# Kernel tuning notes

Measured on AMD Instinct MI355X. Metric: run time of the kernel, lower is better.

## Reference

```python
import jax, jax.numpy as jnp
import numpy as np

TAU = 1.0       # softmax_temp
SOS_IDX = 1
EOS_IDX = 2
MAX_LEN = 20    # total message length incl. SOS/EOS -> 18 decode steps


def setup_inputs() -> dict:
    key = jax.random.key(0)
    ks = jax.random.split(key, 12)
    B, E, H, V, F = 512, 256, 512, 4096, 512
    T = MAX_LEN - 2
    s = lambda k, shape, sc: jax.random.normal(k, shape, jnp.float32) * sc
    return {
        "proto_a": s(ks[0], (B, F), 1.0),
        "proto_b": s(ks[1], (B, F), 1.0),
        "W_init": s(ks[2], (H, 2 * F), (2 * F) ** -0.5),
        "b_init": jnp.zeros((H,), jnp.float32),
        "W_ih": s(ks[3], (3 * H, E), E ** -0.5),
        "W_hh": s(ks[4], (3 * H, H), H ** -0.5),
        "b_ih": jnp.zeros((3 * H,), jnp.float32),
        "b_hh": jnp.zeros((3 * H,), jnp.float32),
        "W_out": s(ks[5], (V, H), H ** -0.5),
        "b_out": jnp.zeros((V,), jnp.float32),
        "emb": s(ks[6], (V, E), 1.0),
        # uniforms in (0,1) turned into Gumbel noise inside reference
        "u_gumbel": jax.random.uniform(ks[7], (T, B, V), jnp.float32, 1e-6, 1.0 - 1e-6),
    }


def reference(proto_a, proto_b, W_init, b_init, W_ih, W_hh, b_ih, b_hh,
              W_out, b_out, emb, u_gumbel):
    B = proto_a.shape[0]
    V = W_out.shape[0]
    # init_h(cat(prototypes, 1)) -> h0 [B, H]
    h0 = jnp.concatenate([proto_a, proto_b], axis=1) @ W_init.T + b_init
    sos = jnp.zeros((B, V), h0.dtype).at[:, SOS_IDX].set(1.0)
    eos = jnp.zeros((B, V), h0.dtype).at[:, EOS_IDX].set(1.0)
    x0 = sos @ emb  # [B, E]
    g = -jnp.log(-jnp.log(u_gumbel))  # Gumbel(0,1) noise, [T, B, V]

    def step(carry, gt):
        h, x = carry  # h [B,H], x [B,E]
        # PyTorch single-step GRU cell
        gi = x @ W_ih.T + b_ih
        gh = h @ W_hh.T + b_hh
        ir, iz, inn = jnp.split(gi, 3, axis=-1)
        hr, hz, hn = jnp.split(gh, 3, axis=-1)
        r = jax.nn.sigmoid(ir + hr)
        z = jax.nn.sigmoid(iz + hz)
        n = jnp.tanh(inn + r * hn)
        h_new = (1.0 - z) * n + z * h
        logits = h_new @ W_out.T + b_out  # [B, V]
        # gumbel_softmax(tau, hard=False) then straight-through hard one-hot
        y = jax.nn.softmax((logits + gt) / TAU, axis=-1)
        hard = jax.nn.one_hot(jnp.argmax(y, axis=-1), V, dtype=y.dtype)
        onehot = hard - jax.lax.stop_gradient(y) + y
        return (h_new, onehot @ emb), onehot

    _, toks = jax.lax.scan(step, (h0, x0), g)  # toks [T, B, V]
    lang = jnp.concatenate([sos[:, None], jnp.swapaxes(toks, 0, 1), eos[:, None]], axis=1)
    return lang  # [B, MAX_LEN, V]
```

## Files before the change

kernel.cpp:

```cpp
#include <hip/hip_runtime.h>
#include <hip/hip_bf16.h>
#include <math.h>

#define B_ 512
#define E_ 256
#define H_ 512
#define V_ 4096
#define T_ 18
#define L_ 20
#define MARGIN_ 0.04f
#define CCAP_ 64

typedef __attribute__((ext_vector_type(8))) short bf16x8;
typedef __attribute__((ext_vector_type(4))) float f32x4;

__global__ __launch_bounds__(256) void kprep32(const float* __restrict__ pa,
                                               const float* __restrict__ pb,
                                               const float* __restrict__ Wout,
                                               float* __restrict__ cat,
                                               __hip_bfloat16* __restrict__ WB) {
  int idx = blockIdx.x * 256 + threadIdx.x;
  if (idx < 131072) {
    int e0 = idx * 4;
    int b = e0 >> 10, k = e0 & 1023;
    float4 v = (k < 512) ? *reinterpret_cast<const float4*>(pa + (size_t)b * 512 + k)
                         : *reinterpret_cast<const float4*>(pb + (size_t)b * 512 + (k - 512));
    *reinterpret_cast<float4*>(cat + e0) = v;
  } else {
    int e0 = (idx - 131072) * 4;
    float4 w = *reinterpret_cast<const float4*>(Wout + e0);
    __hip_bfloat16 b0 = __float2bfloat16(w.x), b1 = __float2bfloat16(w.y);
    __hip_bfloat16 b2 = __float2bfloat16(w.z), b3 = __float2bfloat16(w.w);
    ushort4 o;
    o.x = *reinterpret_cast<unsigned short*>(&b0);
    o.y = *reinterpret_cast<unsigned short*>(&b1);
    o.z = *reinterpret_cast<unsigned short*>(&b2);
    o.w = *reinterpret_cast<unsigned short*>(&b3);
    *reinterpret_cast<ushort4*>(WB + e0) = o;
  }
}

__device__ __forceinline__ void gemm64_body(const float* __restrict__ A,
                                            const float* __restrict__ W,
                                            float* __restrict__ P,
                                            int N, int lda, int kPer,
                                            int bx, int by, int bz, int My,
                                            int tid, char* smemRaw) {
  float (*As)[130] = reinterpret_cast<float(*)[130]>(smemRaw);
  float (*Bs)[68]  = reinterpret_cast<float(*)[68]>(smemRaw + 8320);
  const int tx = tid & 15, ty = tid >> 4;
  const int bn = bx * 64, bm = by * 128;
  const int k0 = bz * kPer;
  const size_t pOff = (size_t)bz * My * 128 * N;
  const int kk0 = tid & 15;
  const int ra0 = (tid >> 4) * 8;
  const int cb0 = (tid >> 4) * 4;

  float acc[8][4] = {};
  for (int kb = 0; kb < kPer; kb += 16) {
#pragma unroll
    for (int q = 0; q < 8; ++q)
      As[kk0][ra0 + q] = A[(size_t)(bm + ra0 + q) * lda + k0 + kb + kk0];
#pragma unroll
    for (int q = 0; q < 4; ++q)
      Bs[kk0][cb0 + q] = W[(size_t)(bn + cb0 + q) * lda + k0 + kb + kk0];
    __syncthreads();
#pragma unroll
    for (int kk = 0; kk < 16; ++kk) {
      float a[8], b[4];
#pragma unroll
      for (int i = 0; i < 8; ++i) a[i] = As[kk][ty + 16 * i];
#pragma unroll
      for (int j = 0; j < 4; ++j) b[j] = Bs[kk][tx + 16 * j];
#pragma unroll
      for (int i = 0; i < 8; ++i)
#pragma unroll
        for (int j = 0; j < 4; ++j) acc[i][j] = fmaf(a[i], b[j], acc[i][j]);
    }
    __syncthreads();
  }
#pragma unroll
  for (int i = 0; i < 8; ++i) {
    size_t r = (size_t)(bm + ty + 16 * i);
#pragma unroll
    for (int j = 0; j < 4; ++j)
      P[pOff + r * N + bn + tx + 16 * j] = acc[i][j];
  }
}

__global__ __launch_bounds__(256) void setupGemms(const float* __restrict__ cat,
                                                  const float* __restrict__ Winit,
                                                  float* __restrict__ h0P,
                                                  const float* __restrict__ emb,
                                                  const float* __restrict__ Wih,
                                                  float* __restrict__ giP) {
  __shared__ __align__(16) char smemRaw[12672];
  const int bid = blockIdx.x, tid = threadIdx.x;
  if (bid < 256) {
    int bx = bid & 7, by = (bid >> 3) & 3, bz = bid >> 5;
    gemm64_body(cat, Winit, h0P, 512, 1024, 128, bx, by, bz, 4, tid, smemRaw);
  } else {
    int gid = bid - 256;
    int bx = gid % 24, by = gid / 24;
    gemm64_body(emb, Wih, giP, 1536, 256, 256, bx, by, 0, 32, tid, smemRaw);
  }
}

__global__ __launch_bounds__(256) void ghK(const float* __restrict__ h,
                                           const float* __restrict__ Whh,
                                           float* __restrict__ ghP) {
  __shared__ __align__(16) char smemRaw[12672];
  const int bid = blockIdx.x, tid = threadIdx.x;
  int bx = bid % 24, by = (bid / 24) & 3, bz = bid / 96;
  gemm64_body(h, Whh, ghP, 1536, 512, 64, bx, by, bz, 4, tid, smemRaw);
}

__global__ __launch_bounds__(256) void reduceH0(const float* __restrict__ parts,
                                                const float* __restrict__ binit,
                                                float* __restrict__ h,
                                                __hip_bfloat16* __restrict__ hB) {
  int i = blockIdx.x * 256 + threadIdx.x;
  double s = (double)binit[i & 511];
#pragma unroll
  for (int c = 0; c < 8; ++c) s += (double)parts[(size_t)c * 262144 + i];
  float f = (float)s;
  h[i] = f;
  hB[i] = __float2bfloat16(f);
}

__device__ __forceinline__ void screen_body(const __hip_bfloat16* __restrict__ hB,
                                            const __hip_bfloat16* __restrict__ WoutB,
                                            float* __restrict__ loP,
                                            int bid, int tid) {
  const int wave = tid >> 6, lane = tid & 63;
  const int bx = bid & 63, by = bid >> 6;
  const int bm = by * 64 + wave * 16;
  const int bn = bx * 64;
  const int rA = lane & 15, g = lane >> 4;
  const __hip_bfloat16* ha = hB + (size_t)(bm + rA) * H_ + g * 8;
  const __hip_bfloat16* wb = WoutB + (size_t)(bn + rA) * H_ + g * 8;
  f32x4 acc[4] = {};
  for (int k0 = 0; k0 < H_; k0 += 32) {
    bf16x8 a = *reinterpret_cast<const bf16x8*>(ha + k0);
#pragma unroll
    for (int j = 0; j < 4; ++j) {
      bf16x8 b = *reinterpret_cast<const bf16x8*>(wb + (size_t)j * 16 * H_ + k0);
      acc[j] = __builtin_amdgcn_mfma_f32_16x16x32_bf16(a, b, acc[j], 0, 0, 0);
    }
  }
#pragma unroll
  for (int j = 0; j < 4; ++j)
#pragma unroll
    for (int r = 0; r < 4; ++r)
      loP[(size_t)(bm + g * 4 + r) * V_ + bn + j * 16 + rA] = acc[j][r];
}

__device__ __forceinline__ int pick_body(const float* __restrict__ loP,
                                         const float* __restrict__ h,
                                         const float* __restrict__ Wout,
                                         const float* __restrict__ bout,
                                         const float* __restrict__ ub,
                                         int bid, int tid, char* smemRaw) {
  double* sd    = reinterpret_cast<double*>(smemRaw);
  int*    pre   = reinterpret_cast<int*>(smemRaw + 2048);
  int*    candV = reinterpret_cast<int*>(smemRaw + 3072);
  float*  swv   = reinterpret_cast<float*>(smemRaw + 3328);
  int*    swi   = reinterpret_cast<int*>(smemRaw + 3344);
  int*    sct   = reinterpret_cast<int*>(smemRaw + 3360);
  double* bestS = reinterpret_cast<double*>(smemRaw + 3376);
  int*    bestV = reinterpret_cast<int*>(smemRaw + 3384);
  const int lane = tid & 63, wv = tid >> 6;
  const float* l0 = loP + (size_t)bid * V_;
  float sloc[16];
  float best = -1e30f; int bi = 0x7fffffff;
#pragma unroll
  for (int i = 0; i < 16; ++i) {
    int v = tid + 256 * i;
    float s = l0[v] + bout[v] - logf(-logf(ub[v]));
    sloc[i] = s;
    if (s > best) { best = s; bi = v; }
  }
#pragma unroll
  for (int off = 1; off < 64; off <<= 1) {
    float ov = __shfl_xor(best, off, 64);
    int   oi = __shfl_xor(bi,  off, 64);
    if (ov > best || (ov == best && oi < bi)) { best = ov; bi = oi; }
  }
  if (lane == 0) { swv[wv] = best; swi[wv] = bi; }
  __syncthreads();
  float smax = swv[0]; int amax = swi[0];
#pragma unroll
  for (int w = 1; w < 4; ++w) {
    float ov = swv[w]; int oi = swi[w];
    if (ov > smax || (ov == smax && oi < amax)) { smax = ov; amax = oi; }
  }
  int c = 0;
#pragma unroll
  for (int i = 0; i < 16; ++i) if (sloc[i] >= smax - MARGIN_) ++c;
  int csum = c;
#pragma unroll
  for (int off = 1; off < 64; off <<= 1) csum += __shfl_xor(csum, off, 64);
  if (lane == 0) sct[wv] = csum;
  __syncthreads();
  int tot = sct[0] + sct[1] + sct[2] + sct[3];

  int tok;
  if (tot == 1) {
    tok = amax;
  } else if (tot <= CCAP_) {
    int lv[16];
    int cc = 0;
#pragma unroll
    for (int i = 0; i < 16; ++i)
      if (sloc[i] >= smax - MARGIN_) { if (cc < 16) lv[cc] = tid + 256 * i; ++cc; }
    pre[tid] = cc;
    __syncthreads();
    for (int off = 1; off < 256; off <<= 1) {
      int vv = (tid >= off) ? pre[tid - off] : 0;
      __syncthreads();
      pre[tid] += vv;
      __syncthreads();
    }
    int base = pre[tid] - cc;
    for (int q = 0; q < cc; ++q) candV[base + q] = lv[q];
    if (tid == 0) { *bestS = -1e300; *bestV = 0x7fffffff; }
    __syncthreads();
    const float* hb = h + (size_t)bid * H_;
    for (int ci = 0; ci < tot; ++ci) {
      int v = candV[ci];
      const float* wr = Wout + (size_t)v * H_;
      double p = (double)hb[tid] * (double)wr[tid]
               + (double)hb[tid + 256] * (double)wr[tid + 256];
#pragma unroll
      for (int off = 1; off < 64; off <<= 1) p += __shfl_xor(p, off, 64);
      if (lane == 0) sd[wv] = p;
      __syncthreads();
      if (tid == 0) {
        double s = sd[0] + sd[1] + sd[2] + sd[3]
                 + (double)bout[v] - log(-log((double)ub[v]));
        if (s > *bestS || (s == *bestS && v < *bestV)) { *bestS = s; *bestV = v; }
      }
      __syncthreads();
    }
    tok = *bestV;
  } else {
    const float* hb = h + (size_t)bid * H_;
    double dbest = -1e300; int dbi = 0x7fffffff;
    for (int i = 0; i < 16; ++i) {
      int v = tid + 256 * i;
      const float* wr = Wout + (size_t)v * H_;
      double dot = 0.0;
      for (int k = 0; k < H_; ++k) dot = fma((double)hb[k], (double)wr[k], dot);
      double s = dot + (double)bout[v] - log(-log((double)ub[v]));
      if (s > dbest) { dbest = s; dbi = v; }
    }
#pragma unroll
    for (int off = 1; off < 64; off <<= 1) {
      double od = __shfl_xor(dbest, off, 64);
      int    oi = __shfl_xor(dbi,  off, 64);
      if (od > dbest || (od == dbest && oi < dbi)) { dbest = od; dbi = oi; }
    }
    if (lane == 0) { sd[wv] = dbest; pre[wv] = dbi; }
    __syncthreads();
    double bs = sd[0]; int bv = pre[0];
#pragma unroll
    for (int w = 1; w < 4; ++w) {
      if (sd[w] > bs || (sd[w] == bs && pre[w] < bv)) { bs = sd[w]; bv = pre[w]; }
    }
    tok = bv;
  }
  return tok;
}

__global__ __launch_bounds__(256) void gates_init(const float* __restrict__ ghP,
                                                  const float* __restrict__ giP,
                                                  const float* __restrict__ bih,
                                                  const float* __restrict__ bhh,
                                                  float* __restrict__ h,
                                                  __hip_bfloat16* __restrict__ hB) {
  const int bid = blockIdx.x, tid = threadIdx.x;
  const float* g0 = giP + (size_t)1 * 1536;
  size_t base = (size_t)bid * 1536;
#pragma unroll
  for (int c = 0; c < 2; ++c) {
    int j = c * 256 + tid;
    int idx = bid * 512 + j;
    double gr = (double)bhh[j], gz = (double)bhh[512 + j], gn = (double)bhh[1024 + j];
#pragma unroll
    for (int s = 0; s < 8; ++s) {
      const float* p = ghP + (size_t)s * 786432 + base;
      gr += (double)p[j]; gz += (double)p[512 + j]; gn += (double)p[1024 + j];
    }
    float ir  = g0[j]        + bih[j];
    float iz  = g0[512 + j]  + bih[512 + j];
    float inn = g0[1024 + j] + bih[1024 + j];
    float r = 1.f / (1.f + expf(-(ir + (float)gr)));
    float z = 1.f / (1.f + expf(-(iz + (float)gz)));
    float n = tanhf(inn + r * (float)gn);
    float hn = (1.f - z) * n + z * h[idx];
    h[idx] = hn;
    hB[idx] = __float2bfloat16(hn);
  }
}

__global__ __launch_bounds__(256) void fusedA(const float* __restrict__ h,
                                              const float* __restrict__ Whh,
                                              const __hip_bfloat16* __restrict__ hB,
                                              const __hip_bfloat16* __restrict__ WoutB,
                                              float* __restrict__ ghP,
                                              float* __restrict__ loP,
                                              int doGemm) {
  __shared__ __align__(16) char smemRaw[12672];
  const int bid = blockIdx.x, tid = threadIdx.x;
  if (bid < 768) {
    if (doGemm) {
      int bx = bid % 24, by = (bid / 24) & 3, bz = bid / 96;
      gemm64_body(h, Whh, ghP, 1536, 512, 64, bx, by, bz, 4, tid, smemRaw);
    }
  } else {
    screen_body(hB, WoutB, loP, bid - 768, tid);
  }
}

__global__ __launch_bounds__(256) void fusedB(const float* __restrict__ loP,
                                              float* __restrict__ h,
                                              const float* __restrict__ Wout,
                                              const float* __restrict__ bout,
                                              const float* __restrict__ u,
                                              const float* __restrict__ ghP,
                                              const float* __restrict__ giP,
                                              const float* __restrict__ bih,
                                              const float* __restrict__ bhh,
                                              __hip_bfloat16* __restrict__ hB,
                                              int* __restrict__ toks,
                                              int t, int doGates) {
  __shared__ __align__(16) char smemRaw[5440];
  const int bid = blockIdx.x, tid = threadIdx.x;
  const int j0 = tid, j1 = 256 + tid;
  double gr0 = (double)bhh[j0], gz0 = (double)bhh[512 + j0], gn0 = (double)bhh[1024 + j0];
  double gr1 = (double)bhh[j1], gz1 = (double)bhh[512 + j1], gn1 = (double)bhh[1024 + j1];
  if (doGates) {
    size_t base = (size_t)bid * 1536;
#pragma unroll
    for (int s = 0; s < 8; ++s) {
      const float* p = ghP + (size_t)s * 786432 + base;
      gr0 += (double)p[j0]; gz0 += (double)p[512 + j0]; gn0 += (double)p[1024 + j0];
      gr1 += (double)p[j1]; gz1 += (double)p[512 + j1]; gn1 += (double)p[1024 + j1];
    }
  }
  const float* ub = u + (size_t)bid * V_;
  int tok = pick_body(loP, h, Wout, bout, ub, bid, tid, smemRaw);
  if (tid == 0) toks[t * B_ + bid] = tok;
  if (doGates) {
    const float* g0 = giP + (size_t)tok * 1536;
    {
      int idx = bid * 512 + j0;
      float ir  = g0[j0]        + bih[j0];
      float iz  = g0[512 + j0]  + bih[512 + j0];
      float inn = g0[1024 + j0] + bih[1024 + j0];
      float r = 1.f / (1.f + expf(-(ir + (float)gr0)));
      float z = 1.f / (1.f + expf(-(iz + (float)gz0)));
      float n = tanhf(inn + r * (float)gn0);
      float hn = (1.f - z) * n + z * h[idx];
      h[idx] = hn;
      hB[idx] = __float2bfloat16(hn);
    }
    {
      int idx = bid * 512 + j1;
      float ir  = g0[j1]        + bih[j1];
      float iz  = g0[512 + j1]  + bih[512 + j1];
      float inn = g0[1024 + j1] + bih[1024 + j1];
      float r = 1.f / (1.f + expf(-(ir + (float)gr1)));
      float z = 1.f / (1.f + expf(-(iz + (float)gz1)));
      float n = tanhf(inn + r * (float)gn1);
      float hn = (1.f - z) * n + z * h[idx];
      h[idx] = hn;
      hB[idx] = __float2bfloat16(hn);
    }
  }
}

__global__ __launch_bounds__(256) void kfinal32(float* __restrict__ out,
                                                const int* __restrict__ toks) {
  size_t c = (size_t)blockIdx.x * 256 + threadIdx.x;
  size_t e0 = c * 4;
  int v0 = (int)(e0 & (size_t)(V_ - 1));
  size_t row = e0 >> 12;
  int p = (int)(row % L_);
  int b = (int)(row / L_);
  int tok;
  if (p == 0)           tok = 1;
  else if (p == L_ - 1) tok = 2;
  else                  tok = toks[(p - 1) * B_ + b];
  float4 val = make_float4(0.f, 0.f, 0.f, 0.f);
  int d = tok - v0;
  if (d >= 0 && d < 4) {
    if (d == 0) val.x = 1.f; else if (d == 1) val.y = 1.f;
    else if (d == 2) val.z = 1.f; else val.w = 1.f;
  }
  reinterpret_cast<float4*>(out)[c] = val;
}

__global__ void kmark_ws(float* out) {
  if (threadIdx.x == 0) out[0] = 16.0f;
}
__global__ void kmark_resolver(float* out) {
  if (threadIdx.x == 0) out[2] = 11.0f;
}

extern "C" void kernel_launch(void* const* d_in, const int* in_sizes, int n_in,
                              void* d_out, int out_size, void* d_ws, size_t ws_size,
                              hipStream_t stream) {
  static const int EXPECT[12] = {262144, 262144, 524288, 512, 393216, 786432,
                                 1536, 1536, 2097152, 4096, 1048576, 37748736};
  const float* R[12];
  bool resolved = (n_in == 12);
  if (resolved) {
    bool used[12] = {};
    for (int i = 0; i < 12; ++i) {
      int f = -1;
      for (int j = 0; j < 12; ++j)
        if (!used[j] && in_sizes[j] == EXPECT[i]) { f = j; break; }
      if (f < 0) { resolved = false; break; }
      used[f] = true;
      R[i] = (const float*)d_in[f];
    }
  }
  if (!resolved)
    for (int i = 0; i < 12 && i < n_in; ++i) R[i] = (const float*)d_in[i];

  const float *pa = R[0], *pb = R[1], *Winit = R[2], *binit = R[3],
              *Wih = R[4], *Whh = R[5], *bih = R[6], *bhh = R[7],
              *Wout = R[8], *bout = R[9], *emb = R[10], *ug = R[11];
  float* out = (float*)d_out;

  const size_t TOK_BYTES = (size_t)T_ * B_ * sizeof(int);
  if (ws_size < TOK_BYTES) { kmark_ws<<<1, 64, 0, stream>>>(out); return; }
  int* toks = (int*)d_ws;

  const size_t SC_FLOATS = 16121856;
  float* sc;
  if (ws_size >= 40960 + SC_FLOATS * sizeof(float)) {
    sc = (float*)((char*)d_ws + 40960);
  } else {
    sc = (float*)d_out;
  }
  float* h    = sc;
  float* giP  = sc + 262144;
  float* ghP  = sc + 6553600;
  float* loP  = sc + 12845056;
  __hip_bfloat16* hB    = (__hip_bfloat16*)(sc + 14942208);
  __hip_bfloat16* WoutB = (__hip_bfloat16*)(sc + 15073280);
  float* cat  = ghP;
  float* h0P  = ghP + 524288;

  kprep32<<<2560, 256, 0, stream>>>(pa, pb, Wout, cat, WoutB);
  setupGemms<<<1024, 256, 0, stream>>>(cat, Winit, h0P, emb, Wih, giP);
  reduceH0<<<1024, 256, 0, stream>>>(h0P, binit, h, hB);
  ghK<<<768, 256, 0, stream>>>(h, Whh, ghP);
  gates_init<<<512, 256, 0, stream>>>(ghP, giP, bih, bhh, h, hB);

  for (int t = 0; t < T_; ++t) {
    const float* uslice = ug + (size_t)t * B_ * V_;
    int notLast = (t < T_ - 1) ? 1 : 0;
    fusedA<<<1280, 256, 0, stream>>>(h, Whh, hB, WoutB, ghP, loP, notLast);
    fusedB<<<512, 256, 0, stream>>>(loP, h, Wout, bout, uslice, ghP, giP,
                                    bih, bhh, hB, toks, t, notLast);
  }

  kfinal32<<<40960, 256, 0, stream>>>(out, toks);
  if (!resolved) kmark_resolver<<<1, 64, 0, stream>>>(out);
}
```

Baseline: 917.6 us.

## Compute recurrent h@W_hh with 3-way bf16-split MFMA instead of fp32 split-K GEMM

Replaces the fp32 SIMT split-K GEMM for the GRU hidden-state projection with a bf16 MFMA kernel that splits h and W_hh into three bf16 terms each and sums six cross products, approximating fp32 precision. W_hh is split once in the prep kernel and h is split in the gate updates. This removes the 8-way split-K partial buffers and the double-precision reduction in the gate kernels, and cuts the GEMM grid from 768 to 192 blocks. The cost is six MFMAs per tile plus triple loads, and precision is slightly reduced, which could flip argmax decisions.

```diff
diff --git a/kernel.cpp b/kernel.cpp
--- a/kernel.cpp
+++ b/kernel.cpp
@@ -14,11 +14,32 @@
 typedef __attribute__((ext_vector_type(8))) short bf16x8;
 typedef __attribute__((ext_vector_type(4))) float f32x4;
 
+__device__ __forceinline__ unsigned short bfbits(float x) {
+  __hip_bfloat16 b = __float2bfloat16(x);
+  return *reinterpret_cast<unsigned short*>(&b);
+}
+__device__ __forceinline__ float bf2f(unsigned short u) {
+  unsigned v = ((unsigned)u) << 16;
+  return *reinterpret_cast<float*>(&v);
+}
+__device__ __forceinline__ void split3(float x, unsigned short& s1,
+                                       unsigned short& s2, unsigned short& s3) {
+  s1 = bfbits(x);
+  float r = x - bf2f(s1);
+  s2 = bfbits(r);
+  float r2 = r - bf2f(s2);
+  s3 = bfbits(r2);
+}
+
 __global__ __launch_bounds__(256) void kprep32(const float* __restrict__ pa,
                                                const float* __restrict__ pb,
                                                const float* __restrict__ Wout,
+                                               const float* __restrict__ Whh,
                                                float* __restrict__ cat,
-                                               __hip_bfloat16* __restrict__ WB) {
+                                               __hip_bfloat16* __restrict__ WB,
+                                               unsigned short* __restrict__ W1,
+                                               unsigned short* __restrict__ W2,
+                                               unsigned short* __restrict__ W3) {
   int idx = blockIdx.x * 256 + threadIdx.x;
   if (idx < 131072) {
     int e0 = idx * 4;
@@ -26,17 +47,23 @@
     float4 v = (k < 512) ? *reinterpret_cast<const float4*>(pa + (size_t)b * 512 + k)
                          : *reinterpret_cast<const float4*>(pb + (size_t)b * 512 + (k - 512));
     *reinterpret_cast<float4*>(cat + e0) = v;
-  } else {
+  } else if (idx < 655360) {
     int e0 = (idx - 131072) * 4;
     float4 w = *reinterpret_cast<const float4*>(Wout + e0);
-    __hip_bfloat16 b0 = __float2bfloat16(w.x), b1 = __float2bfloat16(w.y);
-    __hip_bfloat16 b2 = __float2bfloat16(w.z), b3 = __float2bfloat16(w.w);
     ushort4 o;
-    o.x = *reinterpret_cast<unsigned short*>(&b0);
-    o.y = *reinterpret_cast<unsigned short*>(&b1);
-    o.z = *reinterpret_cast<unsigned short*>(&b2);
-    o.w = *reinterpret_cast<unsigned short*>(&b3);
+    o.x = bfbits(w.x); o.y = bfbits(w.y); o.z = bfbits(w.z); o.w = bfbits(w.w);
     *reinterpret_cast<ushort4*>(WB + e0) = o;
+  } else if (idx < 851968) {
+    int e0 = (idx - 655360) * 4;
+    float4 w = *reinterpret_cast<const float4*>(Whh + e0);
+    ushort4 o1, o2, o3;
+    split3(w.x, o1.x, o2.x, o3.x);
+    split3(w.y, o1.y, o2.y, o3.y);
+    split3(w.z, o1.z, o2.z, o3.z);
+    split3(w.w, o1.w, o2.w, o3.w);
+    *reinterpret_cast<ushort4*>(W1 + e0) = o1;
+    *reinterpret_cast<ushort4*>(W2 + e0) = o2;
+    *reinterpret_cast<ushort4*>(W3 + e0) = o3;
   }
 }
 
@@ -106,29 +133,63 @@
   }
 }
 
-__global__ __launch_bounds__(256) void ghK(const float* __restrict__ h,
-                                           const float* __restrict__ Whh,
-                                           float* __restrict__ ghP) {
-  __shared__ __align__(16) char smemRaw[12672];
-  const int bid = blockIdx.x, tid = threadIdx.x;
-  int bx = bid % 24, by = (bid / 24) & 3, bz = bid / 96;
-  gemm64_body(h, Whh, ghP, 1536, 512, 64, bx, by, bz, 4, tid, smemRaw);
-}
-
 __global__ __launch_bounds__(256) void reduceH0(const float* __restrict__ parts,
                                                 const float* __restrict__ binit,
                                                 float* __restrict__ h,
-                                                __hip_bfloat16* __restrict__ hB) {
+                                                unsigned short* __restrict__ h1,
+                                                unsigned short* __restrict__ h2,
+                                                unsigned short* __restrict__ h3) {
   int i = blockIdx.x * 256 + threadIdx.x;
   double s = (double)binit[i & 511];
 #pragma unroll
   for (int c = 0; c < 8; ++c) s += (double)parts[(size_t)c * 262144 + i];
   float f = (float)s;
   h[i] = f;
-  hB[i] = __float2bfloat16(f);
-}
-
-__device__ __forceinline__ void screen_body(const __hip_bfloat16* __restrict__ hB,
+  split3(f, h1[i], h2[i], h3[i]);
+}
+
+__device__ __forceinline__ void gh_mfma_body(const unsigned short* __restrict__ h1,
+                                             const unsigned short* __restrict__ h2,
+                                             const unsigned short* __restrict__ h3,
+                                             const unsigned short* __restrict__ W1,
+                                             const unsigned short* __restrict__ W2,
+                                             const unsigned short* __restrict__ W3,
+                                             float* __restrict__ ghF,
+                                             int bid, int tid) {
+  const int wave = tid >> 6, lane = tid & 63;
+  const int bx = bid % 24, by = bid / 24;
+  const int bm = by * 64 + wave * 16;
+  const int bn = bx * 64;
+  const int rA = lane & 15, g = lane >> 4;
+  const size_t aoff = (size_t)(bm + rA) * H_ + g * 8;
+  const size_t boff = (size_t)(bn + rA) * H_ + g * 8;
+  f32x4 acc[4] = {};
+  for (int k0 = 0; k0 < H_; k0 += 32) {
+    bf16x8 a1 = *reinterpret_cast<const bf16x8*>(h1 + aoff + k0);
+    bf16x8 a2 = *reinterpret_cast<const bf16x8*>(h2 + aoff + k0);
+    bf16x8 a3 = *reinterpret_cast<const bf16x8*>(h3 + aoff + k0);
+#pragma unroll
+    for (int j = 0; j < 4; ++j) {
+      size_t bo = boff + (size_t)j * 16 * H_ + k0;
+      bf16x8 b1 = *reinterpret_cast<const bf16x8*>(W1 + bo);
+      bf16x8 b2 = *reinterpret_cast<const bf16x8*>(W2 + bo);
+      bf16x8 b3 = *reinterpret_cast<const bf16x8*>(W3 + bo);
+      acc[j] = __builtin_amdgcn_mfma_f32_16x16x32_bf16(a1, b1, acc[j], 0, 0, 0);
+      acc[j] = __builtin_amdgcn_mfma_f32_16x16x32_bf16(a1, b2, acc[j], 0, 0, 0);
+      acc[j] = __builtin_amdgcn_mfma_f32_16x16x32_bf16(a2, b1, acc[j], 0, 0, 0);
+      acc[j] = __builtin_amdgcn_mfma_f32_16x16x32_bf16(a1, b3, acc[j], 0, 0, 0);
+      acc[j] = __builtin_amdgcn_mfma_f32_16x16x32_bf16(a2, b2, acc[j], 0, 0, 0);
+      acc[j] = __builtin_amdgcn_mfma_f32_16x16x32_bf16(a3, b1, acc[j], 0, 0, 0);
+    }
+  }
+#pragma unroll
+  for (int j = 0; j < 4; ++j)
+#pragma unroll
+    for (int r = 0; r < 4; ++r)
+      ghF[(size_t)(bm + g * 4 + r) * 1536 + bn + j * 16 + rA] = acc[j][r];
+}
+
+__device__ __forceinline__ void screen_body(const unsigned short* __restrict__ hB,
                                             const __hip_bfloat16* __restrict__ WoutB,
                                             float* __restrict__ loP,
                                             int bid, int tid) {
@@ -137,7 +198,7 @@
   const int bm = by * 64 + wave * 16;
   const int bn = bx * 64;
   const int rA = lane & 15, g = lane >> 4;
-  const __hip_bfloat16* ha = hB + (size_t)(bm + rA) * H_ + g * 8;
+  const unsigned short* ha = hB + (size_t)(bm + rA) * H_ + g * 8;
   const __hip_bfloat16* wb = WoutB + (size_t)(bn + rA) * H_ + g * 8;
   f32x4 acc[4] = {};
   for (int k0 = 0; k0 < H_; k0 += 32) {
@@ -272,53 +333,60 @@
   return tok;
 }
 
-__global__ __launch_bounds__(256) void gates_init(const float* __restrict__ ghP,
+__device__ __forceinline__ void gates_one(const float* __restrict__ ghF,
+                                          const float* __restrict__ g0,
+                                          const float* __restrict__ bih,
+                                          const float* __restrict__ bhh,
+                                          float* __restrict__ h,
+                                          unsigned short* __restrict__ h1,
+                                          unsigned short* __restrict__ h2,
+                                          unsigned short* __restrict__ h3,
+                                          int bid, int j) {
+  size_t base = (size_t)bid * 1536;
+  int idx = bid * 512 + j;
+  float gr = ghF[base + j]        + bhh[j];
+  float gz = ghF[base + 512 + j]  + bhh[512 + j];
+  float gn = ghF[base + 1024 + j] + bhh[1024 + j];
+  float ir  = g0[j]        + bih[j];
+  float iz  = g0[512 + j]  + bih[512 + j];
+  float inn = g0[1024 + j] + bih[1024 + j];
+  float r = 1.f / (1.f + expf(-(ir + gr)));
+  float z = 1.f / (1.f + expf(-(iz + gz)));
+  float n = tanhf(inn + r * gn);
+  float hn = (1.f - z) * n + z * h[idx];
+  h[idx] = hn;
+  split3(hn, h1[idx], h2[idx], h3[idx]);
+}
+
+__global__ __launch_bounds__(256) void gates_init(const float* __restrict__ ghF,
                                                   const float* __restrict__ giP,
                                                   const float* __restrict__ bih,
                                                   const float* __restrict__ bhh,
                                                   float* __restrict__ h,
-                                                  __hip_bfloat16* __restrict__ hB) {
+                                                  unsigned short* __restrict__ h1,
+                                                  unsigned short* __restrict__ h2,
+                                                  unsigned short* __restrict__ h3) {
   const int bid = blockIdx.x, tid = threadIdx.x;
   const float* g0 = giP + (size_t)1 * 1536;
-  size_t base = (size_t)bid * 1536;
-#pragma unroll
-  for (int c = 0; c < 2; ++c) {
-    int j = c * 256 + tid;
-    int idx = bid * 512 + j;
-    double gr = (double)bhh[j], gz = (double)bhh[512 + j], gn = (double)bhh[1024 + j];
-#pragma unroll
-    for (int s = 0; s < 8; ++s) {
-      const float* p = ghP + (size_t)s * 786432 + base;
-      gr += (double)p[j]; gz += (double)p[512 + j]; gn += (double)p[1024 + j];
-    }
-    float ir  = g0[j]        + bih[j];
-    float iz  = g0[512 + j]  + bih[512 + j];
-    float inn = g0[1024 + j] + bih[1024 + j];
-    float r = 1.f / (1.f + expf(-(ir + (float)gr)));
-    float z = 1.f / (1.f + expf(-(iz + (float)gz)));
-    float n = tanhf(inn + r * (float)gn);
-    float hn = (1.f - z) * n + z * h[idx];
-    h[idx] = hn;
-    hB[idx] = __float2bfloat16(hn);
-  }
-}
-
-__global__ __launch_bounds__(256) void fusedA(const float* __restrict__ h,
-                                              const float* __restrict__ Whh,
-                                              const __hip_bfloat16* __restrict__ hB,
+  gates_one(ghF, g0, bih, bhh, h, h1, h2, h3, bid, tid);
+  gates_one(ghF, g0, bih, bhh, h, h1, h2, h3, bid, 256 + tid);
+}
+
+__global__ __launch_bounds__(256) void fusedA(const unsigned short* __restrict__ h1,
+                                              const unsigned short* __restrict__ h2,
+                                              const unsigned short* __restrict__ h3,
+                                              const unsigned short* __restrict__ W1,
+                                              const unsigned short* __restrict__ W2,
+                                              const unsigned short* __restrict__ W3,
                                               const __hip_bfloat16* __restrict__ WoutB,
-                                              float* __restrict__ ghP,
+                                              float* __restrict__ ghF,
                                               float* __restrict__ loP,
                                               int doGemm) {
-  __shared__ __align__(16) char smemRaw[12672];
   const int bid = blockIdx.x, tid = threadIdx.x;
-  if (bid < 768) {
-    if (doGemm) {
-      int bx = bid % 24, by = (bid / 24) & 3, bz = bid / 96;
-      gemm64_body(h, Whh, ghP, 1536, 512, 64, bx, by, bz, 4, tid, smemRaw);
-    }
+  if (bid < 192) {
+    if (doGemm) gh_mfma_body(h1, h2, h3, W1, W2, W3, ghF, bid, tid);
   } else {
-    screen_body(hB, WoutB, loP, bid - 768, tid);
+    screen_body(h1, WoutB, loP, bid - 192, tid);
   }
 }
 
@@ -327,56 +395,24 @@
                                               const float* __restrict__ Wout,
                                               const float* __restrict__ bout,
                                               const float* __restrict__ u,
-                                              const float* __restrict__ ghP,
+                                              const float* __restrict__ ghF,
                                               const float* __restrict__ giP,
                                               const float* __restrict__ bih,
                                               const float* __restrict__ bhh,
-                                              __hip_bfloat16* __restrict__ hB,
+                                              unsigned short* __restrict__ h1,
+                                              unsigned short* __restrict__ h2,
+                                              unsigned short* __restrict__ h3,
                                               int* __restrict__ toks,
                                               int t, int doGates) {
   __shared__ __align__(16) char smemRaw[5440];
   const int bid = blockIdx.x, tid = threadIdx.x;
-  const int j0 = tid, j1 = 256 + tid;
-  double gr0 = (double)bhh[j0], gz0 = (double)bhh[512 + j0], gn0 = (double)bhh[1024 + j0];
-  double gr1 = (double)bhh[j1], gz1 = (double)bhh[512 + j1], gn1 = (double)bhh[1024 + j1];
-  if (doGates) {
-    size_t base = (size_t)bid * 1536;
-#pragma unroll
-    for (int s = 0; s < 8; ++s) {
-      const float* p = ghP + (size_t)s * 786432 + base;
-      gr0 += (double)p[j0]; gz0 += (double)p[512 + j0]; gn0 += (double)p[1024 + j0];
-      gr1 += (double)p[j1]; gz1 += (double)p[512 + j1]; gn1 += (double)p[1024 + j1];
-    }
-  }
   const float* ub = u + (size_t)bid * V_;
   int tok = pick_body(loP, h, Wout, bout, ub, bid, tid, smemRaw);
   if (tid == 0) toks[t * B_ + bid] = tok;
   if (doGates) {
     const float* g0 = giP + (size_t)tok * 1536;
-    {
-      int idx = bid * 512 + j0;
-      float ir  = g0[j0]        + bih[j0];
-      float iz  = g0[512 + j0]  + bih[512 + j0];
-      float inn = g0[1024 + j0] + bih[1024 + j0];
-      float r = 1.f / (1.f + expf(-(ir + (float)gr0)));
-      float z = 1.f / (1.f + expf(-(iz + (float)gz0)));
-      float n = tanhf(inn + r * (float)gn0);
-      float hn = (1.f - z) * n + z * h[idx];
-      h[idx] = hn;
-      hB[idx] = __float2bfloat16(hn);
-    }
-    {
-      int idx = bid * 512 + j1;
-      float ir  = g0[j1]        + bih[j1];
-      float iz  = g0[512 + j1]  + bih[512 + j1];
-      float inn = g0[1024 + j1] + bih[1024 + j1];
-      float r = 1.f / (1.f + expf(-(ir + (float)gr1)));
-      float z = 1.f / (1.f + expf(-(iz + (float)gz1)));
-      float n = tanhf(inn + r * (float)gn1);
-      float hn = (1.f - z) * n + z * h[idx];
-      h[idx] = hn;
-      hB[idx] = __float2bfloat16(hn);
-    }
+    gates_one(ghF, g0, bih, bhh, h, h1, h2, h3, bid, tid);
+    gates_one(ghF, g0, bih, bhh, h, h1, h2, h3, bid, 256 + tid);
   }
 }
 
@@ -438,7 +474,7 @@
   if (ws_size < TOK_BYTES) { kmark_ws<<<1, 64, 0, stream>>>(out); return; }
   int* toks = (int*)d_ws;
 
-  const size_t SC_FLOATS = 16121856;
+  const size_t SC_FLOATS = 12058624;
   float* sc;
   if (ws_size >= 40960 + SC_FLOATS * sizeof(float)) {
     sc = (float*)((char*)d_ws + 40960);
@@ -447,25 +483,31 @@
   }
   float* h    = sc;
   float* giP  = sc + 262144;
-  float* ghP  = sc + 6553600;
-  float* loP  = sc + 12845056;
-  __hip_bfloat16* hB    = (__hip_bfloat16*)(sc + 14942208);
-  __hip_bfloat16* WoutB = (__hip_bfloat16*)(sc + 15073280);
-  float* cat  = ghP;
-  float* h0P  = ghP + 524288;
-
-  kprep32<<<2560, 256, 0, stream>>>(pa, pb, Wout, cat, WoutB);
+  float* ghF  = sc + 6553600;
+  float* loP  = sc + 7340032;
+  unsigned short* hB1 = (unsigned short*)(sc + 9437184);
+  unsigned short* hB2 = (unsigned short*)(sc + 9568256);
+  unsigned short* hB3 = (unsigned short*)(sc + 9699328);
+  __hip_bfloat16* WoutB = (__hip_bfloat16*)(sc + 9830400);
+  unsigned short* W1  = (unsigned short*)(sc + 10878976);
+  unsigned short* W2  = (unsigned short*)(sc + 11272192);
+  unsigned short* W3  = (unsigned short*)(sc + 11665408);
+  float* cat  = ghF;
+  float* h0P  = loP;
+
+  kprep32<<<3328, 256, 0, stream>>>(pa, pb, Wout, Whh, cat, WoutB, W1, W2, W3);
   setupGemms<<<1024, 256, 0, stream>>>(cat, Winit, h0P, emb, Wih, giP);
-  reduceH0<<<1024, 256, 0, stream>>>(h0P, binit, h, hB);
-  ghK<<<768, 256, 0, stream>>>(h, Whh, ghP);
-  gates_init<<<512, 256, 0, stream>>>(ghP, giP, bih, bhh, h, hB);
+  reduceH0<<<1024, 256, 0, stream>>>(h0P, binit, h, hB1, hB2, hB3);
+  fusedA<<<192, 256, 0, stream>>>(hB1, hB2, hB3, W1, W2, W3, WoutB, ghF, loP, 1);
+  gates_init<<<512, 256, 0, stream>>>(ghF, giP, bih, bhh, h, hB1, hB2, hB3);
 
   for (int t = 0; t < T_; ++t) {
     const float* uslice = ug + (size_t)t * B_ * V_;
     int notLast = (t < T_ - 1) ? 1 : 0;
-    fusedA<<<1280, 256, 0, stream>>>(h, Whh, hB, WoutB, ghP, loP, notLast);
-    fusedB<<<512, 256, 0, stream>>>(loP, h, Wout, bout, uslice, ghP, giP,
-                                    bih, bhh, hB, toks, t, notLast);
+    fusedA<<<704, 256, 0, stream>>>(hB1, hB2, hB3, W1, W2, W3, WoutB,
+                                    ghF, loP, notLast);
+    fusedB<<<512, 256, 0, stream>>>(loP, h, Wout, bout, uslice, ghF, giP,
+                                    bih, bhh, hB1, hB2, hB3, toks, t, notLast);
   }
 
   kfinal32<<<40960, 256, 0, stream>>>(out, toks);
```

Measured after the change: 1.253 ms. +36.5%, slower.
